# Performance work log

Measured on AMD Instinct MI355X. Metric: run time of the kernel, lower is better.

Reference implementation:

```python
import jax, jax.numpy as jnp
import numpy as np

E = 1024
H = 16
D = E // H
B = 4
T = 2048


def setup_inputs() -> dict:
    key = jax.random.key(0)
    ks = jax.random.split(key, 12)
    s = 0.02
    inp = {
        "query": jax.random.normal(ks[0], (B, T, E), jnp.float32),
        "key_in": jax.random.normal(ks[1], (B, T, E), jnp.float32),
        "value": jax.random.normal(ks[2], (B, T, E), jnp.float32),
        "mask": jnp.tril(jnp.ones((T, T), jnp.int32))[None, None, :, :],
        "Wq": jax.random.normal(ks[3], (E, E), jnp.float32) * s,
        "bq": jnp.zeros((E,), jnp.float32),
        "Wk": jax.random.normal(ks[4], (E, E), jnp.float32) * s,
        "bk": jnp.zeros((E,), jnp.float32),
        "Wv": jax.random.normal(ks[5], (E, E), jnp.float32) * s,
        "bv": jnp.zeros((E,), jnp.float32),
        "Wo": jax.random.normal(ks[6], (E, E), jnp.float32) * s,
        "bo": jnp.zeros((E,), jnp.float32),
    }
    return inp


def _shape(x):
    # [B, T, E] -> [B, H, T, D]
    return x.reshape(B, -1, H, D).transpose(0, 2, 1, 3)


def reference(query, key_in, value, mask, Wq, bq, Wk, bk, Wv, bv, Wo, bo):
    q = _shape(query @ Wq.T + bq)
    k = _shape(key_in @ Wk.T + bk)
    v = _shape(value @ Wv.T + bv)
    scale = 1.0 / jnp.sqrt(jnp.float32(D))
    # [B, H, Tq, Tk]
    scores = jnp.einsum("bhqd,bhkd->bhqk", q, k) * scale
    scores = jnp.where(mask == 0, jnp.float32(-jnp.inf), scores)
    attn = jax.nn.softmax(scores, axis=-1)
    out = jnp.einsum("bhqk,bhkd->bhqd", attn, v)
    out = out.transpose(0, 2, 1, 3).reshape(B, T, E)
    return out @ Wo.T + bo
```

## Files before the change

### kernel.cpp

```cpp
#include <hip/hip_runtime.h>
#include <hip/hip_bf16.h>
#include <cstdint>

#define BB 4
#define TT 2048
#define EE 1024
#define HH 16
#define DD 64
#define BH (BB*HH)
#define MM (BB*TT)
#define KK 1024
#define KSTR 72
#define VSTR 136
#define LOG2E 1.44269504088896340736f

typedef __attribute__((ext_vector_type(8))) short short8;
typedef __attribute__((ext_vector_type(4))) short short4_;
typedef __attribute__((ext_vector_type(4))) float float4_;
typedef __attribute__((ext_vector_type(4))) ushort ushort4_;

__device__ __forceinline__ void gl_lds16(const void* g, void* l) {
    __builtin_amdgcn_global_load_lds(
        (const __attribute__((address_space(1))) void*)g,
        (__attribute__((address_space(3))) void*)l, 16, 0, 0);
}

__device__ __forceinline__ ushort f2bf(float v) {
    __hip_bfloat16 h = __float2bfloat16(v);
    return *(ushort*)&h;
}

__global__ __launch_bounds__(256) void cvt_kernel(
    const float* __restrict__ s0, ushort* __restrict__ d0, int n0,
    const float* __restrict__ s1, ushort* __restrict__ d1, int n1,
    const float* __restrict__ s2, ushort* __restrict__ d2, int n2,
    const float* __restrict__ s3, ushort* __restrict__ d3, int n3)
{
    const float* s; ushort* d; int n;
    switch (blockIdx.y) {
        case 0: s = s0; d = d0; n = n0; break;
        case 1: s = s1; d = d1; n = n1; break;
        case 2: s = s2; d = d2; n = n2; break;
        default: s = s3; d = d3; n = n3; break;
    }
    int i = (blockIdx.x * 256 + threadIdx.x) * 4;
    if (i >= n) return;
    float4_ v = *(const float4_*)&s[i];
    ushort4_ o;
#pragma unroll
    for (int j = 0; j < 4; j++) o[j] = f2bf(v[j]);
    *(ushort4_*)&d[i] = o;
}

__global__ __launch_bounds__(256, 3) void gemm_qkv(
    const float* __restrict__ Aq, const float* __restrict__ Ak,
    const float* __restrict__ Av,
    const ushort* __restrict__ Wqc, const ushort* __restrict__ Wkc,
    const ushort* __restrict__ Wvc,
    const float* __restrict__ bq, const float* __restrict__ bk,
    const float* __restrict__ bv,
    ushort* __restrict__ Oq, ushort* __restrict__ Ok, ushort* __restrict__ Ov,
    float qscale)
{
    __shared__ __align__(16) float  Asf[128*32];
    __shared__ __align__(16) ushort Bs [128*32];

    const int bid = blockIdx.x;
    const int swz = (bid & 7) * 192 + (bid >> 3);
    const int z   = swz >> 9;
    const int rem = swz & 511;
    const int bx  = rem & 7;
    const int by  = rem >> 3;

    const float*  A    = (z == 0) ? Aq  : (z == 1) ? Ak  : Av;
    const ushort* W    = (z == 0) ? Wqc : (z == 1) ? Wkc : Wvc;
    const float*  bias = (z == 0) ? bq  : (z == 1) ? bk  : bv;
    ushort*       Cout = (z == 0) ? Oq  : (z == 1) ? Ok  : Ov;
    const float   scale = (z == 0) ? qscale : 1.0f;
    const bool    modeT = (z == 2);

    const int tid  = threadIdx.x;
    const int wave = tid >> 6;
    const int lane = tid & 63;
    const int l15  = lane & 15;
    const int quad = lane >> 4;
    const int wm   = wave & 1;
    const int wn   = wave >> 1;

    const long rowBase = (long)by * 128;
    const long colBase = (long)bx * 128;

    float4_ acc[4][4];
#pragma unroll
    for (int i = 0; i < 4; i++)
#pragma unroll
        for (int j = 0; j < 4; j++) acc[i][j] = float4_{0.f, 0.f, 0.f, 0.f};

    for (int k0 = 0; k0 < KK; k0 += 32) {
        __syncthreads();
#pragma unroll
        for (int it = 0; it < 4; it++) {
            int idx = it * 256 + tid;
            int r = idx >> 3, c = idx & 7;
            int csrc = c ^ (r & 7);
            gl_lds16(A + (rowBase + r) * KK + k0 + csrc * 4, &Asf[idx * 4]);
        }
#pragma unroll
        for (int it = 0; it < 2; it++) {
            int idx = it * 256 + tid;
            int r = idx >> 2, c8 = (idx & 3) * 8;
            gl_lds16(W + (colBase + r) * KK + k0 + c8, &Bs[idx * 8]);
        }
        __syncthreads();

        short8 af[4], bf[4];
#pragma unroll
        for (int mt = 0; mt < 4; mt++) {
            const int r = wm*64 + mt*16 + l15;
            const int s = r & 7;
            const float* arow = &Asf[r * 32];
            float4_ a0 = *(const float4_*)&arow[((2*quad    ) ^ s) * 4];
            float4_ a1 = *(const float4_*)&arow[((2*quad + 1) ^ s) * 4];
#pragma unroll
            for (int j = 0; j < 4; j++) {
                af[mt][j]     = (short)f2bf(a0[j]);
                af[mt][j + 4] = (short)f2bf(a1[j]);
            }
        }
#pragma unroll
        for (int nt = 0; nt < 4; nt++)
            bf[nt] = *(const short8*)&Bs[(wn*64 + nt*16 + l15) * 32 + quad*8];
#pragma unroll
        for (int mt = 0; mt < 4; mt++)
#pragma unroll
            for (int nt = 0; nt < 4; nt++)
                acc[mt][nt] = __builtin_amdgcn_mfma_f32_16x16x32_bf16(
                    af[mt], bf[nt], acc[mt][nt], 0, 0, 0);
    }

#pragma unroll
    for (int nt = 0; nt < 4; nt++) {
        const long col = colBase + wn*64 + nt*16 + l15;
        const float bvv = bias[col];
        const long h = col >> 6, d = col & (DD - 1);
#pragma unroll
        for (int mt = 0; mt < 4; mt++) {
            const long row0 = rowBase + wm*64 + mt*16 + quad*4;
            if (modeT) {
                const long b = row0 >> 11, t0 = row0 & (TT - 1);
                ushort4_ pk;
#pragma unroll
                for (int i = 0; i < 4; i++) pk[i] = f2bf((acc[mt][nt][i] + bvv) * scale);
                *(ushort4_*)&Cout[((b*HH + h)*DD + d)*TT + t0] = pk;
            } else {
#pragma unroll
                for (int i = 0; i < 4; i++) {
                    const long row = row0 + i;
                    const long b = row >> 11, t = row & (TT - 1);
                    Cout[(((b*HH + h) * TT) + t) * DD + d] =
                        f2bf((acc[mt][nt][i] + bvv) * scale);
                }
            }
        }
    }
}

__global__ __launch_bounds__(256, 3) void gemm_out(
    const ushort* __restrict__ A, const ushort* __restrict__ W,
    const float* __restrict__ bias, float* __restrict__ Cout)
{
    __shared__ __align__(16) ushort As[128*32];
    __shared__ __align__(16) ushort Bs[128*32];

    const int bid = blockIdx.x;
    const int swz = (bid & 7) * 64 + (bid >> 3);
    const int bx  = swz & 7;
    const int by  = swz >> 3;

    const int tid  = threadIdx.x;
    const int wave = tid >> 6;
    const int lane = tid & 63;
    const int l15  = lane & 15;
    const int quad = lane >> 4;
    const int wm   = wave & 1;
    const int wn   = wave >> 1;

    const long rowBase = (long)by * 128;
    const long colBase = (long)bx * 128;

    float4_ acc[4][4];
#pragma unroll
    for (int i = 0; i < 4; i++)
#pragma unroll
        for (int j = 0; j < 4; j++) acc[i][j] = float4_{0.f, 0.f, 0.f, 0.f};

    for (int k0 = 0; k0 < KK; k0 += 32) {
        __syncthreads();
#pragma unroll
        for (int it = 0; it < 2; it++) {
            int idx = it * 256 + tid;
            int r   = idx >> 2;
            int c8  = (idx & 3) * 8;
            gl_lds16(A + (rowBase + r) * KK + k0 + c8, &As[idx * 8]);
            gl_lds16(W + (colBase + r) * KK + k0 + c8, &Bs[idx * 8]);
        }
        __syncthreads();

        short8 af[4], bf[4];
#pragma unroll
        for (int mt = 0; mt < 4; mt++)
            af[mt] = *(const short8*)&As[(wm*64 + mt*16 + l15) * 32 + quad*8];
#pragma unroll
        for (int nt = 0; nt < 4; nt++)
            bf[nt] = *(const short8*)&Bs[(wn*64 + nt*16 + l15) * 32 + quad*8];
#pragma unroll
        for (int mt = 0; mt < 4; mt++)
#pragma unroll
            for (int nt = 0; nt < 4; nt++)
                acc[mt][nt] = __builtin_amdgcn_mfma_f32_16x16x32_bf16(
                    af[mt], bf[nt], acc[mt][nt], 0, 0, 0);
    }

#pragma unroll
    for (int nt = 0; nt < 4; nt++) {
        const long col = colBase + wn*64 + nt*16 + l15;
        const float bv = bias[col];
#pragma unroll
        for (int mt = 0; mt < 4; mt++) {
            const long row0 = rowBase + wm*64 + mt*16 + quad*4;
#pragma unroll
            for (int i = 0; i < 4; i++)
                Cout[(row0 + i) * EE + col] = acc[mt][nt][i] + bv;
        }
    }
}

__global__ __launch_bounds__(512, 4) void flash_kernel(
    const ushort* __restrict__ Qh, const ushort* __restrict__ Kh,
    const ushort* __restrict__ Vt, ushort* __restrict__ AO)
{
    __shared__ __align__(16) ushort Ks[2][128*KSTR];
    __shared__ __align__(16) ushort Vs[2][64*VSTR];

    const int p   = blockIdx.x;
    const int bh  = blockIdx.y;
    const int tid = threadIdx.x;
    const int wave = tid >> 6, lane = tid & 63;
    const int l15 = lane & 15, quad = lane >> 4;

    const ushort* Qb = Qh + (long)bh * TT * DD;
    const ushort* Kb = Kh + (long)bh * TT * DD;
    const ushort* Vb = Vt + (long)bh * DD * TT;
    const int h = bh & (HH - 1);
    const int b = bh >> 4;

    int kks[2], kss[2], dds[2], vss[2];
#pragma unroll
    for (int it = 0; it < 2; it++) {
        int c = it * 512 + tid;
        kks[it] = c >> 3; kss[it] = c & 7;
        dds[it] = c >> 4; vss[it] = c & 15;
    }

#pragma unroll
    for (int seg = 0; seg < 2; seg++) {
        const int qt  = (seg == 0) ? (15 - p) : p;
        const int nkt = qt + 1;

        const int qrow = qt*128 + wave*16 + l15;
        short8 aq0 = *(const short8*)&Qb[(long)qrow * DD + quad*8];
        short8 aq1 = *(const short8*)&Qb[(long)qrow * DD + 32 + quad*8];

        float4_ o[4];
#pragma unroll
        for (int nt = 0; nt < 4; nt++) o[nt] = float4_{0.f, 0.f, 0.f, 0.f};
        float m_run = -INFINITY, l_run = 0.0f;

        short8 kreg[2], vreg[2];
#pragma unroll
        for (int it = 0; it < 2; it++) {
            kreg[it] = *(const short8*)&Kb[(long)kks[it] * DD + kss[it]*8];
            vreg[it] = *(const short8*)&Vb[(long)dds[it] * TT + vss[it]*8];
        }
        __syncthreads();
#pragma unroll
        for (int it = 0; it < 2; it++) {
            *(short8*)&Ks[0][kks[it]*KSTR + kss[it]*8] = kreg[it];
            *(short8*)&Vs[0][dds[it]*VSTR + vss[it]*8] = vreg[it];
        }
        __syncthreads();
        int cur = 0;

        for (int kt = 0; kt < nkt; kt++) {
            if (kt + 1 < nkt) {
                const long koff = (long)(kt+1) * 128;
#pragma unroll
                for (int it = 0; it < 2; it++) {
                    kreg[it] = *(const short8*)&Kb[(koff + kks[it]) * DD + kss[it]*8];
                    vreg[it] = *(const short8*)&Vb[(long)dds[it] * TT + koff + vss[it]*8];
                }
            }
            const ushort* ksb = &Ks[cur][0];
            const ushort* vsb = &Vs[cur][0];

            float4_ s[8];
            __builtin_amdgcn_s_setprio(1);
#pragma unroll
            for (int nt = 0; nt < 8; nt++) {
                short8 bk0 = *(const short8*)&ksb[(nt*16 + l15) * KSTR + quad*8];
                short8 bk1 = *(const short8*)&ksb[(nt*16 + l15) * KSTR + 32 + quad*8];
                float4_ acc = float4_{0.f, 0.f, 0.f, 0.f};
                acc = __builtin_amdgcn_mfma_f32_16x16x32_bf16(bk0, aq0, acc, 0,0,0);
                acc = __builtin_amdgcn_mfma_f32_16x16x32_bf16(bk1, aq1, acc, 0,0,0);
                s[nt] = acc;
            }
            __builtin_amdgcn_s_setprio(0);

            if (kt == nkt - 1) {
#pragma unroll
                for (int nt = 0; nt < 8; nt++) {
#pragma unroll
                    for (int i = 0; i < 4; i++) {
                        const int key = kt*128 + nt*16 + quad*4 + i;
                        if (key > qrow) s[nt][i] = -INFINITY;
                    }
                }
            }

            float t8[8];
#pragma unroll
            for (int nt = 0; nt < 8; nt++)
                t8[nt] = fmaxf(fmaxf(s[nt][0], s[nt][1]), fmaxf(s[nt][2], s[nt][3]));
            float pm = fmaxf(fmaxf(fmaxf(t8[0], t8[1]), fmaxf(t8[2], t8[3])),
                             fmaxf(fmaxf(t8[4], t8[5]), fmaxf(t8[6], t8[7])));
            pm = fmaxf(pm, __shfl_xor(pm, 16));
            pm = fmaxf(pm, __shfl_xor(pm, 32));

            if (!__all(pm <= m_run + 8.0f)) {
                const float mnew = fmaxf(m_run, pm);
                const float alpha = exp2f(m_run - mnew);
                m_run = mnew;
                l_run *= alpha;
#pragma unroll
                for (int nt = 0; nt < 4; nt++)
#pragma unroll
                    for (int i = 0; i < 4; i++) o[nt][i] *= alpha;
            }

            float rs0 = 0.f, rs1 = 0.f, rs2 = 0.f, rs3 = 0.f;
            short8 pb[4];
#pragma unroll
            for (int c = 0; c < 4; c++) {
#pragma unroll
                for (int half = 0; half < 2; half++) {
                    const int nt = 2*c + half;
                    const float p0 = exp2f(s[nt][0] - m_run);
                    const float p1 = exp2f(s[nt][1] - m_run);
                    const float p2 = exp2f(s[nt][2] - m_run);
                    const float p3 = exp2f(s[nt][3] - m_run);
                    rs0 += p0; rs1 += p1; rs2 += p2; rs3 += p3;
                    pb[c][half*4 + 0] = (short)f2bf(p0);
                    pb[c][half*4 + 1] = (short)f2bf(p1);
                    pb[c][half*4 + 2] = (short)f2bf(p2);
                    pb[c][half*4 + 3] = (short)f2bf(p3);
                }
            }
            float rs = (rs0 + rs1) + (rs2 + rs3);
            rs += __shfl_xor(rs, 16);
            rs += __shfl_xor(rs, 32);
            l_run += rs;

            __builtin_amdgcn_s_setprio(1);
#pragma unroll
            for (int c = 0; c < 4; c++) {
                const short8 bp = pb[c];
#pragma unroll
                for (int nt = 0; nt < 4; nt++) {
                    const ushort* vrow = &vsb[(nt*16 + l15) * VSTR];
                    short4_ lo = *(const short4_*)&vrow[(2*c    )*16 + quad*4];
                    short4_ hi = *(const short4_*)&vrow[(2*c + 1)*16 + quad*4];
                    short8 av;
                    av[0]=lo[0]; av[1]=lo[1]; av[2]=lo[2]; av[3]=lo[3];
                    av[4]=hi[0]; av[5]=hi[1]; av[6]=hi[2]; av[7]=hi[3];
                    o[nt] = __builtin_amdgcn_mfma_f32_16x16x32_bf16(av, bp, o[nt], 0,0,0);
                }
            }
            __builtin_amdgcn_s_setprio(0);

            if (kt + 1 < nkt) {
#pragma unroll
                for (int it = 0; it < 2; it++) {
                    *(short8*)&Ks[cur^1][kks[it]*KSTR + kss[it]*8] = kreg[it];
                    *(short8*)&Vs[cur^1][dds[it]*VSTR + vss[it]*8] = vreg[it];
                }
                __syncthreads();
                cur ^= 1;
            }
        }

        const float inv = 1.0f / l_run;
        const long rowOff = ((long)(b*TT + qrow)) * EE + h*64;
#pragma unroll
        for (int nt = 0; nt < 4; nt++) {
            ushort4_ pk;
#pragma unroll
            for (int i = 0; i < 4; i++) pk[i] = f2bf(o[nt][i] * inv);
            *(ushort4_*)&AO[rowOff + nt*16 + quad*4] = pk;
        }
    }
}

extern "C" void kernel_launch(void* const* d_in, const int* in_sizes, int n_in,
                              void* d_out, int out_size, void* d_ws, size_t ws_size,
                              hipStream_t stream)
{
    const float* query  = (const float*)d_in[0];
    const float* key_in = (const float*)d_in[1];
    const float* value  = (const float*)d_in[2];
    const float* Wq = (const float*)d_in[4];
    const float* bq = (const float*)d_in[5];
    const float* Wk = (const float*)d_in[6];
    const float* bk = (const float*)d_in[7];
    const float* Wv = (const float*)d_in[8];
    const float* bv = (const float*)d_in[9];
    const float* Wo = (const float*)d_in[10];
    const float* bo = (const float*)d_in[11];

    ushort* ws = (ushort*)d_ws;
    const size_t NIN = (size_t)MM * KK;
    const size_t NW  = (size_t)EE * KK;
    ushort* Wqc = ws;
    ushort* Wkc = Wqc + NW;
    ushort* Wvc = Wkc + NW;
    ushort* Woc = Wvc + NW;
    ushort* Qh  = Woc + NW;
    ushort* Kh  = Qh + NIN;
    ushort* Vth = Kh + NIN;
    ushort* AO  = Vth + NIN;

    const dim3 cvtW_grid(NW/1024, 4);

    cvt_kernel<<<cvtW_grid, 256, 0, stream>>>(Wq, Wqc, (int)NW, Wk, Wkc, (int)NW,
                                              Wv, Wvc, (int)NW, Wo, Woc, (int)NW);

    gemm_qkv<<<dim3(3 * (EE/128) * (MM/128)), 256, 0, stream>>>(
        query, key_in, value, Wqc, Wkc, Wvc, bq, bk, bv, Qh, Kh, Vth,
        0.125f * LOG2E);

    flash_kernel<<<dim3(8, BH), 512, 0, stream>>>(Qh, Kh, Vth, AO);

    gemm_out<<<dim3((EE/128) * (MM/128)), 256, 0, stream>>>(AO, Woc, bo, (float*)d_out);
}
```

Before: 361.1 us.

## Double-buffer LDS tiles in QKV and output projection GEMMs

Both projection GEMMs now keep two LDS buffers and issue the async global-to-LDS loads for the next K tile before computing on the current one. Each iteration then uses a single vmcnt wait plus barrier instead of two syncthreads. This aims to hide global load latency behind MFMA work. The cost is doubled shared memory per block, which could limit occupancy.

New measurement: 394.4 us. +9.2%, slower.

```diff
diff --git a/kernel.cpp b/kernel.cpp
--- a/kernel.cpp
+++ b/kernel.cpp
@@ -62,8 +62,8 @@
     ushort* __restrict__ Oq, ushort* __restrict__ Ok, ushort* __restrict__ Ov,
     float qscale)
 {
-    __shared__ __align__(16) float  Asf[128*32];
-    __shared__ __align__(16) ushort Bs [128*32];
+    __shared__ __align__(16) float  Asf[2][128*32];
+    __shared__ __align__(16) ushort Bs [2][128*32];
 
     const int bid = blockIdx.x;
     const int swz = (bid & 7) * 192 + (bid >> 3);
@@ -90,35 +90,43 @@
     const long rowBase = (long)by * 128;
     const long colBase = (long)bx * 128;
 
-    float4_ acc[4][4];
-#pragma unroll
-    for (int i = 0; i < 4; i++)
-#pragma unroll
-        for (int j = 0; j < 4; j++) acc[i][j] = float4_{0.f, 0.f, 0.f, 0.f};
-
-    for (int k0 = 0; k0 < KK; k0 += 32) {
-        __syncthreads();
+    auto STAGE = [&](int buf, int k0) {
 #pragma unroll
         for (int it = 0; it < 4; it++) {
             int idx = it * 256 + tid;
             int r = idx >> 3, c = idx & 7;
             int csrc = c ^ (r & 7);
-            gl_lds16(A + (rowBase + r) * KK + k0 + csrc * 4, &Asf[idx * 4]);
+            gl_lds16(A + (rowBase + r) * KK + k0 + csrc * 4, &Asf[buf][idx * 4]);
         }
 #pragma unroll
         for (int it = 0; it < 2; it++) {
             int idx = it * 256 + tid;
             int r = idx >> 2, c8 = (idx & 3) * 8;
-            gl_lds16(W + (colBase + r) * KK + k0 + c8, &Bs[idx * 8]);
-        }
-        __syncthreads();
+            gl_lds16(W + (colBase + r) * KK + k0 + c8, &Bs[buf][idx * 8]);
+        }
+    };
+
+    float4_ acc[4][4];
+#pragma unroll
+    for (int i = 0; i < 4; i++)
+#pragma unroll
+        for (int j = 0; j < 4; j++) acc[i][j] = float4_{0.f, 0.f, 0.f, 0.f};
+
+    STAGE(0, 0);
+    asm volatile("s_waitcnt vmcnt(0)" ::: "memory");
+    __builtin_amdgcn_s_barrier();
+
+    const int NT = KK / 32;
+    for (int t = 0; t < NT; t++) {
+        const int cur = t & 1;
+        if (t + 1 < NT) STAGE(cur ^ 1, (t + 1) * 32);
 
         short8 af[4], bf[4];
 #pragma unroll
         for (int mt = 0; mt < 4; mt++) {
             const int r = wm*64 + mt*16 + l15;
             const int s = r & 7;
-            const float* arow = &Asf[r * 32];
+            const float* arow = &Asf[cur][r * 32];
             float4_ a0 = *(const float4_*)&arow[((2*quad    ) ^ s) * 4];
             float4_ a1 = *(const float4_*)&arow[((2*quad + 1) ^ s) * 4];
 #pragma unroll
@@ -129,13 +137,18 @@
         }
 #pragma unroll
         for (int nt = 0; nt < 4; nt++)
-            bf[nt] = *(const short8*)&Bs[(wn*64 + nt*16 + l15) * 32 + quad*8];
+            bf[nt] = *(const short8*)&Bs[cur][(wn*64 + nt*16 + l15) * 32 + quad*8];
 #pragma unroll
         for (int mt = 0; mt < 4; mt++)
 #pragma unroll
             for (int nt = 0; nt < 4; nt++)
                 acc[mt][nt] = __builtin_amdgcn_mfma_f32_16x16x32_bf16(
                     af[mt], bf[nt], acc[mt][nt], 0, 0, 0);
+
+        if (t + 1 < NT) {
+            asm volatile("s_waitcnt vmcnt(0)" ::: "memory");
+            __builtin_amdgcn_s_barrier();
+        }
     }
 
 #pragma unroll
@@ -169,8 +182,8 @@
     const ushort* __restrict__ A, const ushort* __restrict__ W,
     const float* __restrict__ bias, float* __restrict__ Cout)
 {
-    __shared__ __align__(16) ushort As[128*32];
-    __shared__ __align__(16) ushort Bs[128*32];
+    __shared__ __align__(16) ushort As[2][128*32];
+    __shared__ __align__(16) ushort Bs[2][128*32];
 
     const int bid = blockIdx.x;
     const int swz = (bid & 7) * 64 + (bid >> 3);
@@ -188,37 +201,50 @@
     const long rowBase = (long)by * 128;
     const long colBase = (long)bx * 128;
 
-    float4_ acc[4][4];
-#pragma unroll
-    for (int i = 0; i < 4; i++)
-#pragma unroll
-        for (int j = 0; j < 4; j++) acc[i][j] = float4_{0.f, 0.f, 0.f, 0.f};
-
-    for (int k0 = 0; k0 < KK; k0 += 32) {
-        __syncthreads();
+    auto STAGE = [&](int buf, int k0) {
 #pragma unroll
         for (int it = 0; it < 2; it++) {
             int idx = it * 256 + tid;
             int r   = idx >> 2;
             int c8  = (idx & 3) * 8;
-            gl_lds16(A + (rowBase + r) * KK + k0 + c8, &As[idx * 8]);
-            gl_lds16(W + (colBase + r) * KK + k0 + c8, &Bs[idx * 8]);
-        }
-        __syncthreads();
+            gl_lds16(A + (rowBase + r) * KK + k0 + c8, &As[buf][idx * 8]);
+            gl_lds16(W + (colBase + r) * KK + k0 + c8, &Bs[buf][idx * 8]);
+        }
+    };
+
+    float4_ acc[4][4];
+#pragma unroll
+    for (int i = 0; i < 4; i++)
+#pragma unroll
+        for (int j = 0; j < 4; j++) acc[i][j] = float4_{0.f, 0.f, 0.f, 0.f};
+
+    STAGE(0, 0);
+    asm volatile("s_waitcnt vmcnt(0)" ::: "memory");
+    __builtin_amdgcn_s_barrier();
+
+    const int NT = KK / 32;
+    for (int t = 0; t < NT; t++) {
+        const int cur = t & 1;
+        if (t + 1 < NT) STAGE(cur ^ 1, (t + 1) * 32);
 
         short8 af[4], bf[4];
 #pragma unroll
         for (int mt = 0; mt < 4; mt++)
-            af[mt] = *(const short8*)&As[(wm*64 + mt*16 + l15) * 32 + quad*8];
+            af[mt] = *(const short8*)&As[cur][(wm*64 + mt*16 + l15) * 32 + quad*8];
 #pragma unroll
         for (int nt = 0; nt < 4; nt++)
-            bf[nt] = *(const short8*)&Bs[(wn*64 + nt*16 + l15) * 32 + quad*8];
+            bf[nt] = *(const short8*)&Bs[cur][(wn*64 + nt*16 + l15) * 32 + quad*8];
 #pragma unroll
         for (int mt = 0; mt < 4; mt++)
 #pragma unroll
             for (int nt = 0; nt < 4; nt++)
                 acc[mt][nt] = __builtin_amdgcn_mfma_f32_16x16x32_bf16(
                     af[mt], bf[nt], acc[mt][nt], 0, 0, 0);
+
+        if (t + 1 < NT) {
+            asm volatile("s_waitcnt vmcnt(0)" ::: "memory");
+            __builtin_amdgcn_s_barrier();
+        }
     }
 
 #pragma unroll
```
